# Performance work log

Hardware: AMD Instinct MI355X
Metric: run time of the kernel (lower is better)

Reference implementation:

```python
import jax, jax.numpy as jnp
import numpy as np

HIDDEN = 1024
BATCH = 8192
N_STEPS = 50


def setup_inputs() -> dict:
    key = jax.random.key(0)
    k1, k2, k3 = jax.random.split(key, 3)
    x0 = jax.random.normal(k1, (HIDDEN, BATCH), dtype=jnp.float32)
    W = jax.random.normal(k2, (HIDDEN, HIDDEN), dtype=jnp.float32) * (1.0 / np.sqrt(HIDDEN))
    b = jax.random.normal(k3, (HIDDEN, 1), dtype=jnp.float32)
    t0 = jnp.zeros((), dtype=jnp.float32)
    t1 = jnp.ones((), dtype=jnp.float32)
    return {"x0": x0, "t0": t0, "t1": t1, "W": W, "b": b}


def reference(x0, t0, t1, W, b):
    # Euler integration: x_{i+1} = x_i + h * (W @ x_i + b), h = (t1 - t0) / N
    h = (t1 - t0) / N_STEPS

    def step(x, _):
        x = x + h * (W @ x + b)  # b [H,1] broadcasts over batch
        return x, None

    x_final, _ = jax.lax.scan(step, x0, None, length=N_STEPS)
    return x_final
```

## Files before the change

kernel.cpp:

```cpp
#include <hip/hip_runtime.h>

#define H 1024
#define HH (H * H)
#define BATCH 8192
#define NSTEPS 50

typedef __attribute__((ext_vector_type(8))) short bf16x8;
typedef __attribute__((ext_vector_type(4))) float f32x4;

__device__ __forceinline__ void split2(float a, unsigned short& h, unsigned short& l)
{
    unsigned u = __float_as_uint(a);
    float r = a - __uint_as_float(u & 0xFFFF0000u);
    h = (unsigned short)(u >> 16);
    l = (unsigned short)((__float_as_uint(r) + 0x8000u) >> 16);
}
__device__ __forceinline__ unsigned short rnd_bf16(float a)
{
    return (unsigned short)((__float_as_uint(a) + 0x8000u) >> 16);
}
__device__ __forceinline__ float bf2f(unsigned short s)
{
    return __uint_as_float(((unsigned)s) << 16);
}
__device__ __forceinline__ void gload16(const void* g, void* l)
{
    __builtin_amdgcn_global_load_lds(
        (const __attribute__((address_space(1))) void*)g,
        (__attribute__((address_space(3))) void*)l, 16, 0, 0);
}
#define VMCNT(n) asm volatile("s_waitcnt vmcnt(" #n ")" ::: "memory")
#define RBAR() do { __builtin_amdgcn_s_barrier(); __builtin_amdgcn_sched_barrier(0); } while (0)

__global__ void setup_k(const float* __restrict__ W, const float* __restrict__ bvec,
                        const float* __restrict__ t0, const float* __restrict__ t1,
                        unsigned short* __restrict__ Aplanes,
                        float* __restrict__ cv, float* __restrict__ v0)
{
    __shared__ unsigned short th[64][68], tl[64][68];
    const float h = (t1[0] - t0[0]) / (float)NSTEPS;
    const int bid = blockIdx.x, tid = threadIdx.x;
    const int rb = (bid >> 4) * 64, cb = (bid & 15) * 64;
    const int row = tid >> 2, c16 = (tid & 3) * 16;

    unsigned short* Ahi  = Aplanes;
    unsigned short* Alo  = Aplanes + HH;
    unsigned short* AhiT = Aplanes + 2 * HH;
    unsigned short* AloT = Aplanes + 3 * HH;

    {
        const float* wsrc = &W[(size_t)(rb + row) * H + cb + c16];
        bf16x8 hv[2], lv[2];
        #pragma unroll
        for (int q = 0; q < 16; ++q) {
            const float a = h * wsrc[q] + ((rb + row) == (cb + c16 + q) ? 1.0f : 0.0f);
            unsigned short hh, ll;
            split2(a, hh, ll);
            hv[q >> 3][q & 7] = (short)hh;
            lv[q >> 3][q & 7] = (short)ll;
            th[row][c16 + q] = hh;
            tl[row][c16 + q] = ll;
        }
        *(bf16x8*)&Ahi[(size_t)(rb + row) * H + cb + c16] = hv[0];
        *(bf16x8*)&Ahi[(size_t)(rb + row) * H + cb + c16 + 8] = hv[1];
        *(bf16x8*)&Alo[(size_t)(rb + row) * H + cb + c16] = lv[0];
        *(bf16x8*)&Alo[(size_t)(rb + row) * H + cb + c16 + 8] = lv[1];
    }
    __syncthreads();
    {
        bf16x8 hv[2], lv[2];
        #pragma unroll
        for (int q = 0; q < 16; ++q) {
            hv[q >> 3][q & 7] = (short)th[c16 + q][row];
            lv[q >> 3][q & 7] = (short)tl[c16 + q][row];
        }
        *(bf16x8*)&AhiT[(size_t)(cb + row) * H + rb + c16] = hv[0];
        *(bf16x8*)&AhiT[(size_t)(cb + row) * H + rb + c16 + 8] = hv[1];
        *(bf16x8*)&AloT[(size_t)(cb + row) * H + rb + c16] = lv[0];
        *(bf16x8*)&AloT[(size_t)(cb + row) * H + rb + c16 + 8] = lv[1];
    }
    if (bid == 0) {
        #pragma unroll
        for (int rep = 0; rep < 4; ++rep) {
            const int i = tid + rep * 256;
            const float v = h * bvec[i];
            cv[i] = v; v0[i] = v;
        }
    }
}

template<bool WRITE_N, bool WRITE_T, bool DO_X, bool PR>
__launch_bounds__(512)
__global__ void chain_fused_k(const unsigned short* __restrict__ Lhi,
                              const unsigned short* __restrict__ Llo,
                              const unsigned short* __restrict__ RThi,
                              const unsigned short* __restrict__ RTlo,
                              unsigned short* __restrict__ Qhi,
                              unsigned short* __restrict__ Qlo,
                              unsigned short* __restrict__ QhiT,
                              unsigned short* __restrict__ QloT,
                              const float* __restrict__ vin,
                              const float* __restrict__ addv,
                              float* __restrict__ vout,
                              const float* __restrict__ X,
                              unsigned short* __restrict__ XhiT)
{
    __shared__ unsigned short sA[2][2][2][64][32];
    __shared__ unsigned short sB[2][2][2][64][32];

    const int tid = threadIdx.x;
    const int bid = blockIdx.x;
    const int wave = tid >> 6, lane = tid & 63;

    if (DO_X && bid >= 272) {
        float (*ts)[65] = (float(*)[65])&sA[0][0][0][0][0];
        const int tile = bid - 272;
        const int n0x = (tile >> 4) * 64, k0x = (tile & 15) * 64;
        #pragma unroll
        for (int p = 0; p < 2; ++p) {
            const int kr = p * 32 + (tid >> 4);
            const int c4 = (tid & 15) * 4;
            const float4 v = *(const float4*)&X[(size_t)(k0x + kr) * BATCH + n0x + c4];
            ts[kr][c4 + 0] = v.x; ts[kr][c4 + 1] = v.y;
            ts[kr][c4 + 2] = v.z; ts[kr][c4 + 3] = v.w;
        }
        __syncthreads();
        {
            const int n = tid >> 3;
            const int kc = (tid & 7) * 8;
            bf16x8 hv;
            #pragma unroll
            for (int q = 0; q < 8; ++q)
                hv[q] = (short)rnd_bf16(ts[kc + q][n]);
            *(bf16x8*)&XhiT[(size_t)(n0x + n) * H + k0x + kc] = hv;
        }
        return;
    }

    if (bid >= 256) {
        const int rowbase = (bid - 256) * 64 + wave * 8;
        const float4* xq = (const float4*)vin + lane * 4;
        float4 xv[4];
        #pragma unroll
        for (int q = 0; q < 4; ++q) xv[q] = xq[q];
        #pragma unroll
        for (int rr = 0; rr < 8; ++rr) {
            const int row = rowbase + rr;
            const unsigned short* mh = Lhi + (size_t)row * H + lane * 16;
            const unsigned short* ml = Llo + (size_t)row * H + lane * 16;
            bf16x8 h0 = *(const bf16x8*)&mh[0];
            bf16x8 h1 = *(const bf16x8*)&mh[8];
            bf16x8 l0 = *(const bf16x8*)&ml[0];
            bf16x8 l1 = *(const bf16x8*)&ml[8];
            float s = 0.0f;
            #pragma unroll
            for (int q = 0; q < 8; ++q) {
                const float m0v = bf2f((unsigned short)h0[q]) + bf2f((unsigned short)l0[q]);
                const float m1v = bf2f((unsigned short)h1[q]) + bf2f((unsigned short)l1[q]);
                const float* xf = (const float*)xv;
                s = fmaf(m0v, xf[q], s);
                s = fmaf(m1v, xf[8 + q], s);
            }
            #pragma unroll
            for (int off = 32; off; off >>= 1)
                s += __shfl_down(s, off, 64);
            if (lane == 0) vout[row] = addv[row] + s;
        }
        return;
    }

    const int lg = lane >> 4, lm = lane & 15;
    const int half = wave >> 2;
    const int wq = wave & 3;
    const int wr2 = (wq >> 1) * 32, wc2 = (wq & 1) * 32;
    const int xcd = bid & 7;
    const int idx0 = bid >> 3;
    const int mt = (xcd >> 1) * 4 + (idx0 & 3);
    const int nt = (xcd & 1) * 8 + (idx0 >> 2);
    const int m0 = mt * 64, n0 = nt * 64;

    f32x4 acc[2][2] = {};

    #define CSTAGE(tt, b) do {                                                   \
        _Pragma("unroll")                                                        \
        for (int it = 0; it < 4; ++it) {                                         \
            const int idx = tid + it * 512;                                      \
            const int mat = idx >> 10, kh = (idx >> 9) & 1;                      \
            const int plane = (idx >> 8) & 1;                                    \
            const int row = (idx >> 2) & 63, kc = idx & 3;                       \
            const int ks = kc ^ ((row >> 1) & 3);                                \
            const unsigned short* g = mat ? (plane ? RTlo : RThi)                \
                                          : (plane ? Llo : Lhi);                 \
            const int rb = mat ? n0 : m0;                                        \
            unsigned short* d = mat ? &sB[b][kh][plane][row][kc * 8]             \
                                    : &sA[b][kh][plane][row][kc * 8];            \
            gload16(g + (size_t)(rb + row) * H + kh * 512 + (tt) * 32 + ks * 8, d); \
        }                                                                        \
    } while (0)

    CSTAGE(0, 0);
    __syncthreads();
    int buf = 0;
    for (int t = 0; t < 16; ++t) {
        if (t + 1 < 16) CSTAGE(t + 1, buf ^ 1);
        bf16x8 ah[2], al[2], bh[2], bl[2];
        #pragma unroll
        for (int i = 0; i < 2; ++i) {
            const int row = wr2 + i * 16 + lm;
            const int sl = lg ^ ((row >> 1) & 3);
            ah[i] = *(const bf16x8*)&sA[buf][half][0][row][sl * 8];
            al[i] = *(const bf16x8*)&sA[buf][half][1][row][sl * 8];
            const int rn = wc2 + i * 16 + lm;
            const int sn = lg ^ ((rn >> 1) & 3);
            bh[i] = *(const bf16x8*)&sB[buf][half][0][rn][sn * 8];
            bl[i] = *(const bf16x8*)&sB[buf][half][1][rn][sn * 8];
        }
        #pragma unroll
        for (int i = 0; i < 2; ++i)
            #pragma unroll
            for (int j = 0; j < 2; ++j) {
                acc[i][j] = __builtin_amdgcn_mfma_f32_16x16x32_bf16(ah[i], bh[j], acc[i][j], 0, 0, 0);
                acc[i][j] = __builtin_amdgcn_mfma_f32_16x16x32_bf16(ah[i], bl[j], acc[i][j], 0, 0, 0);
                acc[i][j] = __builtin_amdgcn_mfma_f32_16x16x32_bf16(al[i], bh[j], acc[i][j], 0, 0, 0);
            }
        __syncthreads();
        buf ^= 1;
    }
    #undef CSTAGE

    float* red = (float*)&sA[0][0][0][0][0];
    const int ridx = wq * 64 + lane;
    if (half == 1) {
        float* dst = red + (size_t)ridx * 17;
        #pragma unroll
        for (int i = 0; i < 2; ++i)
            #pragma unroll
            for (int j = 0; j < 2; ++j)
                *(f32x4*)&dst[(i * 2 + j) * 4] = acc[i][j];
    }
    __syncthreads();
    if (half == 0) {
        const float* src = red + (size_t)ridx * 17;
        #pragma unroll
        for (int i = 0; i < 2; ++i)
            #pragma unroll
            for (int j = 0; j < 2; ++j) {
                const f32x4 p = *(const f32x4*)&src[(i * 2 + j) * 4];
                acc[i][j] += p;
            }
        #pragma unroll
        for (int i = 0; i < 2; ++i) {
            const int row0 = m0 + wr2 + i * 16 + lg * 4;
            #pragma unroll
            for (int j = 0; j < 2; ++j) {
                const int col = n0 + wc2 + j * 16 + lm;
                if (PR) {
                    #pragma unroll
                    for (int r = 0; r < 4; ++r)
                        Qhi[(size_t)(row0 + r) * H + col] = rnd_bf16(acc[i][j][r]);
                } else {
                    unsigned short hs[4], ls[4];
                    #pragma unroll
                    for (int r = 0; r < 4; ++r) {
                        split2(acc[i][j][r], hs[r], ls[r]);
                        if (WRITE_N) {
                            Qhi[(size_t)(row0 + r) * H + col] = hs[r];
                            Qlo[(size_t)(row0 + r) * H + col] = ls[r];
                        }
                    }
                    if (WRITE_T) {
                        ushort4 th, tl;
                        th.x = hs[0]; th.y = hs[1]; th.z = hs[2]; th.w = hs[3];
                        tl.x = ls[0]; tl.y = ls[1]; tl.z = ls[2]; tl.w = ls[3];
                        *(ushort4*)&QhiT[(size_t)col * H + row0] = th;
                        *(ushort4*)&QloT[(size_t)col * H + row0] = tl;
                    }
                }
            }
        }
    }
}

__launch_bounds__(256)
__global__ void big_gemm1_k(const unsigned short* __restrict__ Pr,
                            const unsigned short* __restrict__ XhiT,
                            float* __restrict__ C, const float* __restrict__ bias)
{
    __shared__ unsigned short sA[3][128][32];
    __shared__ unsigned short sB[3][128][32];

    const int tid = threadIdx.x;
    const int wave = tid >> 6, lane = tid & 63;
    const int lg = lane >> 4, lm = lane & 15;
    const int wr2 = (wave >> 1) * 64;
    const int wc2 = (wave & 1) * 64;
    const int bid = blockIdx.x;
    const int l = bid >> 3;
    const int m0 = (l & 7) * 128;
    const int n0 = ((bid & 7) * 8 + (l >> 3)) * 128;

    f32x4 acc[4][4] = {};

    #define BSTAGE(tt, b) do {                                                   \
        _Pragma("unroll")                                                        \
        for (int it = 0; it < 2; ++it) {                                         \
            const int idx = tid + it * 256;                                      \
            const int row = idx >> 2, kc = idx & 3;                              \
            const int ks = kc ^ ((row >> 1) & 3);                                \
            const size_t go = (size_t)(tt) * 32 + ks * 8;                        \
            gload16(Pr   + (size_t)(m0 + row) * H + go, &sA[b][row][kc * 8]);    \
            gload16(XhiT + (size_t)(n0 + row) * H + go, &sB[b][row][kc * 8]);    \
        }                                                                        \
    } while (0)

    BSTAGE(0, 0);
    BSTAGE(1, 1);
    VMCNT(2);
    RBAR();

    #pragma unroll
    for (int t = 0; t < 32; ++t) {
        const int b = t % 3;
        bf16x8 ah[4], bh[4];
        #pragma unroll
        for (int i = 0; i < 4; ++i) {
            const int row = wr2 + i * 16 + lm;
            const int sl = lg ^ ((row >> 1) & 3);
            ah[i] = *(const bf16x8*)&sA[b][row][sl * 8];
            const int rn = wc2 + i * 16 + lm;
            const int sn = lg ^ ((rn >> 1) & 3);
            bh[i] = *(const bf16x8*)&sB[b][rn][sn * 8];
        }
        if (t + 2 < 32) BSTAGE(t + 2, (t + 2) % 3);
        __builtin_amdgcn_s_setprio(1);
        #pragma unroll
        for (int i = 0; i < 4; ++i)
            #pragma unroll
            for (int j = 0; j < 4; ++j)
                acc[i][j] = __builtin_amdgcn_mfma_f32_16x16x32_bf16(ah[i], bh[j], acc[i][j], 0, 0, 0);
        __builtin_amdgcn_s_setprio(0);
        if (t < 30) VMCNT(2);
        else if (t == 30) VMCNT(0);
        if (t < 31) RBAR();
    }
    #undef BSTAGE

    #pragma unroll
    for (int i = 0; i < 4; ++i) {
        const int row0 = m0 + wr2 + i * 16 + lg * 4;
        #pragma unroll
        for (int r = 0; r < 4; ++r) {
            const float bv = bias[row0 + r];
            float* dst = &C[(size_t)(row0 + r) * BATCH + n0 + wc2 + lm];
            #pragma unroll
            for (int j = 0; j < 4; ++j)
                dst[j * 16] = acc[i][j][r] + bv;
        }
    }
}

#define PADK 40

__launch_bounds__(256)
__global__ void big_gemm_k(const unsigned short* __restrict__ Ahi_g,
                           const unsigned short* __restrict__ Alo_g,
                           const float* __restrict__ X, float* __restrict__ C,
                           const float* __restrict__ bias)
{
    __shared__ unsigned short Ahi[128][PADK], Alo[128][PADK];
    __shared__ unsigned short Bhi[128][PADK], Blo[128][PADK];

    const int tid = threadIdx.x;
    const int wave = tid >> 6;
    const int lane = tid & 63;
    const int wr = (wave >> 1) * 64;
    const int wc = (wave & 1) * 64;
    const int m0 = blockIdx.y * 128;
    const int n0 = blockIdx.x * 128;
    const int lg = lane >> 4;
    const int lm = lane & 15;

    f32x4 acc[4][4] = {};

    for (int k0 = 0; k0 < H; k0 += 32) {
        #pragma unroll
        for (int a2 = 0; a2 < 2; ++a2) {
            const int id = tid + a2 * 256;
            const int row = id >> 2;
            const int ko = id & 3;
            const size_t g = (size_t)(m0 + row) * H + k0 + ko * 8;
            *(bf16x8*)&Ahi[row][ko * 8] = *(const bf16x8*)&Ahi_g[g];
            *(bf16x8*)&Alo[row][ko * 8] = *(const bf16x8*)&Alo_g[g];
        }
        #pragma unroll
        for (int a2 = 0; a2 < 2; ++a2) {
            const int id = tid + a2 * 256;
            const int n = id & 127;
            const int ko = id >> 7;
            const float* src = &X[(size_t)(k0 + ko * 8) * BATCH + n0 + n];
            bf16x8 bh, bl;
            #pragma unroll
            for (int i = 0; i < 8; ++i) {
                unsigned short hh, ll;
                split2(src[(size_t)i * BATCH], hh, ll);
                bh[i] = (short)hh;
                bl[i] = (short)ll;
            }
            *(bf16x8*)&Bhi[n][ko * 8] = bh;
            *(bf16x8*)&Blo[n][ko * 8] = bl;
        }
        __syncthreads();

        bf16x8 ah[4], al[4], bh[4], bl[4];
        #pragma unroll
        for (int i = 0; i < 4; ++i) {
            const int m = wr + i * 16 + lm;
            ah[i] = *(const bf16x8*)&Ahi[m][lg * 8];
            al[i] = *(const bf16x8*)&Alo[m][lg * 8];
            const int n = wc + i * 16 + lm;
            bh[i] = *(const bf16x8*)&Bhi[n][lg * 8];
            bl[i] = *(const bf16x8*)&Blo[n][lg * 8];
        }
        #pragma unroll
        for (int i = 0; i < 4; ++i)
            #pragma unroll
            for (int j = 0; j < 4; ++j) {
                acc[i][j] = __builtin_amdgcn_mfma_f32_16x16x32_bf16(ah[i], bh[j], acc[i][j], 0, 0, 0);
                acc[i][j] = __builtin_amdgcn_mfma_f32_16x16x32_bf16(ah[i], bl[j], acc[i][j], 0, 0, 0);
                acc[i][j] = __builtin_amdgcn_mfma_f32_16x16x32_bf16(al[i], bh[j], acc[i][j], 0, 0, 0);
            }
        __syncthreads();
    }

    #pragma unroll
    for (int i = 0; i < 4; ++i) {
        const int rowb = m0 + wr + i * 16 + lg * 4;
        #pragma unroll
        for (int r = 0; r < 4; ++r) {
            const float bv = bias[rowb + r];
            float* dst = &C[(size_t)(rowb + r) * BATCH + n0 + wc + lm];
            #pragma unroll
            for (int j = 0; j < 4; ++j)
                dst[j * 16] = acc[i][j][r] + bv;
        }
    }
}

extern "C" void kernel_launch(void* const* d_in, const int* in_sizes, int n_in,
                              void* d_out, int out_size, void* d_ws, size_t ws_size,
                              hipStream_t stream)
{
    const float* x0 = (const float*)d_in[0];
    const float* t0 = (const float*)d_in[1];
    const float* t1 = (const float*)d_in[2];
    const float* W  = (const float*)d_in[3];
    const float* bb = (const float*)d_in[4];
    float* out = (float*)d_out;

    unsigned short* Aplanes = (unsigned short*)d_ws;
    unsigned short* Ahi  = Aplanes;
    unsigned short* Alo  = Aplanes + HH;
    float* cv = (float*)(Aplanes + 4 * HH);
    float* v0 = cv + H;
    float* v1 = v0 + H;

    const size_t xtoff = (size_t)16 * 1024 * 1024;
    const bool useXT = ws_size >= xtoff + (size_t)BATCH * H * sizeof(unsigned short);
    unsigned short* XhiT = (unsigned short*)((char*)d_ws + xtoff);

    unsigned short* PA = (unsigned short*)d_out;
    unsigned short* PB = PA + (size_t)4 * HH;

    setup_k<<<256, 256, 0, stream>>>(W, bb, t0, t1, Aplanes, cv, v0);

    const int seq[7] = {0, 1, 0, 0, 0, 1, 0};
    unsigned short* cur = Ahi;
    float* vin = v0;
    float* vout = v1;
    for (int s = 0; s < 7; ++s) {
        const unsigned short* L  = seq[s] ? Ahi : cur;
        const unsigned short* Ll = seq[s] ? Alo : cur + HH;
        const float* addv = seq[s] ? cv : vin;
        if (s == 0) {
            unsigned short* nxt = PA;
            if (useXT) {
                chain_fused_k<false, true, true, false><<<2320, 512, 0, stream>>>(
                    L, Ll, cur + 2 * HH, cur + 3 * HH,
                    nxt, nxt + HH, nxt + 2 * HH, nxt + 3 * HH,
                    vin, addv, vout, x0, XhiT);
            } else {
                chain_fused_k<false, true, false, false><<<272, 512, 0, stream>>>(
                    L, Ll, cur + 2 * HH, cur + 3 * HH,
                    nxt, nxt + HH, nxt + 2 * HH, nxt + 3 * HH,
                    vin, addv, vout, nullptr, nullptr);
            }
            cur = nxt;
        } else if (s == 4) {
            unsigned short* nxt = PA;
            chain_fused_k<false, true, false, false><<<272, 512, 0, stream>>>(
                L, Ll, cur + 2 * HH, cur + 3 * HH,
                nxt, nxt + HH, nxt + 2 * HH, nxt + 3 * HH,
                vin, addv, vout, nullptr, nullptr);
            cur = nxt;
        } else if (s < 6) {
            unsigned short* nxt = (s & 1) ? PB : PA;
            chain_fused_k<true, true, false, false><<<272, 512, 0, stream>>>(
                L, Ll, cur + 2 * HH, cur + 3 * HH,
                nxt, nxt + HH, nxt + 2 * HH, nxt + 3 * HH,
                vin, addv, vout, nullptr, nullptr);
            cur = nxt;
        } else if (useXT) {
            chain_fused_k<false, false, false, true><<<272, 512, 0, stream>>>(
                L, Ll, cur + 2 * HH, cur + 3 * HH,
                Ahi, nullptr, nullptr, nullptr,
                vin, addv, vout, nullptr, nullptr);
            cur = Ahi;
        } else {
            chain_fused_k<true, false, false, false><<<272, 512, 0, stream>>>(
                L, Ll, cur + 2 * HH, cur + 3 * HH,
                Ahi, Alo, nullptr, nullptr,
                vin, addv, vout, nullptr, nullptr);
            cur = Ahi;
        }
        float* tv = vin; vin = vout; vout = tv;
    }

    if (useXT) {
        big_gemm1_k<<<512, 256, 0, stream>>>(Ahi, XhiT, out, vin);
    } else {
        big_gemm_k<<<dim3(BATCH / 128, H / 128), 256, 0, stream>>>(
            Ahi, Alo, x0, out, vin);
    }
}
```

Measured before the change: 150.8 us.

## Fold matvec into GEMM blocks, add BK64 chain tiles, deepen big GEMM prefetch

```diff
diff --git a/kernel.cpp b/kernel.cpp
--- a/kernel.cpp
+++ b/kernel.cpp
@@ -89,7 +89,7 @@
     }
 }
 
-template<bool WRITE_N, bool WRITE_T, bool DO_X, bool PR>
+template<bool WRITE_N, bool WRITE_T, bool DO_X, bool PR, bool BK64>
 __launch_bounds__(512)
 __global__ void chain_fused_k(const unsigned short* __restrict__ Lhi,
                               const unsigned short* __restrict__ Llo,
@@ -105,16 +105,20 @@
                               const float* __restrict__ X,
                               unsigned short* __restrict__ XhiT)
 {
-    __shared__ unsigned short sA[2][2][2][64][32];
-    __shared__ unsigned short sB[2][2][2][64][32];
+    constexpr int BKH = BK64 ? 64 : 32;
+    constexpr int NIT = 512 / BKH;
+    constexpr int GPR = BKH / 8;
+
+    __shared__ unsigned short sA[2][2][2][64][BKH];
+    __shared__ unsigned short sB[2][2][2][64][BKH];
 
     const int tid = threadIdx.x;
     const int bid = blockIdx.x;
     const int wave = tid >> 6, lane = tid & 63;
 
-    if (DO_X && bid >= 272) {
+    if (DO_X && bid >= 256) {
         float (*ts)[65] = (float(*)[65])&sA[0][0][0][0][0];
-        const int tile = bid - 272;
+        const int tile = bid - 256;
         const int n0x = (tile >> 4) * 64, k0x = (tile & 15) * 64;
         #pragma unroll
         for (int p = 0; p < 2; ++p) {
@@ -133,38 +137,6 @@
             for (int q = 0; q < 8; ++q)
                 hv[q] = (short)rnd_bf16(ts[kc + q][n]);
             *(bf16x8*)&XhiT[(size_t)(n0x + n) * H + k0x + kc] = hv;
-        }
-        return;
-    }
-
-    if (bid >= 256) {
-        const int rowbase = (bid - 256) * 64 + wave * 8;
-        const float4* xq = (const float4*)vin + lane * 4;
-        float4 xv[4];
-        #pragma unroll
-        for (int q = 0; q < 4; ++q) xv[q] = xq[q];
-        #pragma unroll
-        for (int rr = 0; rr < 8; ++rr) {
-            const int row = rowbase + rr;
-            const unsigned short* mh = Lhi + (size_t)row * H + lane * 16;
-            const unsigned short* ml = Llo + (size_t)row * H + lane * 16;
-            bf16x8 h0 = *(const bf16x8*)&mh[0];
-            bf16x8 h1 = *(const bf16x8*)&mh[8];
-            bf16x8 l0 = *(const bf16x8*)&ml[0];
-            bf16x8 l1 = *(const bf16x8*)&ml[8];
-            float s = 0.0f;
-            #pragma unroll
-            for (int q = 0; q < 8; ++q) {
-                const float m0v = bf2f((unsigned short)h0[q]) + bf2f((unsigned short)l0[q]);
-                const float m1v = bf2f((unsigned short)h1[q]) + bf2f((unsigned short)l1[q]);
-                const float* xf = (const float*)xv;
-                s = fmaf(m0v, xf[q], s);
-                s = fmaf(m1v, xf[8 + q], s);
-            }
-            #pragma unroll
-            for (int off = 32; off; off >>= 1)
-                s += __shfl_down(s, off, 64);
-            if (lane == 0) vout[row] = addv[row] + s;
         }
         return;
     }
@@ -181,48 +153,54 @@
 
     f32x4 acc[2][2] = {};
 
-    #define CSTAGE(tt, b) do {                                                   \
-        _Pragma("unroll")                                                        \
-        for (int it = 0; it < 4; ++it) {                                         \
-            const int idx = tid + it * 512;                                      \
-            const int mat = idx >> 10, kh = (idx >> 9) & 1;                      \
-            const int plane = (idx >> 8) & 1;                                    \
-            const int row = (idx >> 2) & 63, kc = idx & 3;                       \
-            const int ks = kc ^ ((row >> 1) & 3);                                \
-            const unsigned short* g = mat ? (plane ? RTlo : RThi)                \
-                                          : (plane ? Llo : Lhi);                 \
-            const int rb = mat ? n0 : m0;                                        \
-            unsigned short* d = mat ? &sB[b][kh][plane][row][kc * 8]             \
-                                    : &sA[b][kh][plane][row][kc * 8];            \
-            gload16(g + (size_t)(rb + row) * H + kh * 512 + (tt) * 32 + ks * 8, d); \
-        }                                                                        \
+    #define CSTAGE(tt, b) do {                                                     \
+        _Pragma("unroll")                                                          \
+        for (int it = 0; it < GPR; ++it) {                                         \
+            const int idx = tid + it * 512;                                        \
+            const int kc = idx % GPR;                                              \
+            const int row = (idx / GPR) & 63;                                      \
+            const int plane = (idx / (GPR * 64)) & 1;                              \
+            const int kh = (idx / (GPR * 128)) & 1;                                \
+            const int mat = idx / (GPR * 256);                                     \
+            const int ks = BK64 ? (kc ^ (row & 7)) : (kc ^ ((row >> 1) & 3));      \
+            const unsigned short* g = mat ? (plane ? RTlo : RThi)                  \
+                                          : (plane ? Llo : Lhi);                   \
+            const int rb = mat ? n0 : m0;                                          \
+            unsigned short* d = mat ? &sB[b][kh][plane][row][kc * 8]               \
+                                    : &sA[b][kh][plane][row][kc * 8];              \
+            gload16(g + (size_t)(rb + row) * H + kh * 512 + (tt) * BKH + ks * 8, d); \
+        }                                                                          \
     } while (0)
 
     CSTAGE(0, 0);
     __syncthreads();
     int buf = 0;
-    for (int t = 0; t < 16; ++t) {
-        if (t + 1 < 16) CSTAGE(t + 1, buf ^ 1);
-        bf16x8 ah[2], al[2], bh[2], bl[2];
-        #pragma unroll
-        for (int i = 0; i < 2; ++i) {
-            const int row = wr2 + i * 16 + lm;
-            const int sl = lg ^ ((row >> 1) & 3);
-            ah[i] = *(const bf16x8*)&sA[buf][half][0][row][sl * 8];
-            al[i] = *(const bf16x8*)&sA[buf][half][1][row][sl * 8];
-            const int rn = wc2 + i * 16 + lm;
-            const int sn = lg ^ ((rn >> 1) & 3);
-            bh[i] = *(const bf16x8*)&sB[buf][half][0][rn][sn * 8];
-            bl[i] = *(const bf16x8*)&sB[buf][half][1][rn][sn * 8];
-        }
-        #pragma unroll
-        for (int i = 0; i < 2; ++i)
-            #pragma unroll
-            for (int j = 0; j < 2; ++j) {
-                acc[i][j] = __builtin_amdgcn_mfma_f32_16x16x32_bf16(ah[i], bh[j], acc[i][j], 0, 0, 0);
-                acc[i][j] = __builtin_amdgcn_mfma_f32_16x16x32_bf16(ah[i], bl[j], acc[i][j], 0, 0, 0);
-                acc[i][j] = __builtin_amdgcn_mfma_f32_16x16x32_bf16(al[i], bh[j], acc[i][j], 0, 0, 0);
+    for (int t = 0; t < NIT; ++t) {
+        if (t + 1 < NIT) CSTAGE(t + 1, buf ^ 1);
+        #pragma unroll
+        for (int kk = 0; kk < (BK64 ? 2 : 1); ++kk) {
+            bf16x8 ah[2], al[2], bh[2], bl[2];
+            #pragma unroll
+            for (int i = 0; i < 2; ++i) {
+                const int row = wr2 + i * 16 + lm;
+                const int g = kk * 4 + lg;
+                const int sl = BK64 ? (g ^ (row & 7)) : (g ^ ((row >> 1) & 3));
+                ah[i] = *(const bf16x8*)&sA[buf][half][0][row][sl * 8];
+                al[i] = *(const bf16x8*)&sA[buf][half][1][row][sl * 8];
+                const int rn = wc2 + i * 16 + lm;
+                const int sn = BK64 ? (g ^ (rn & 7)) : (g ^ ((rn >> 1) & 3));
+                bh[i] = *(const bf16x8*)&sB[buf][half][0][rn][sn * 8];
+                bl[i] = *(const bf16x8*)&sB[buf][half][1][rn][sn * 8];
             }
+            #pragma unroll
+            for (int i = 0; i < 2; ++i)
+                #pragma unroll
+                for (int j = 0; j < 2; ++j) {
+                    acc[i][j] = __builtin_amdgcn_mfma_f32_16x16x32_bf16(ah[i], bh[j], acc[i][j], 0, 0, 0);
+                    acc[i][j] = __builtin_amdgcn_mfma_f32_16x16x32_bf16(ah[i], bl[j], acc[i][j], 0, 0, 0);
+                    acc[i][j] = __builtin_amdgcn_mfma_f32_16x16x32_bf16(al[i], bh[j], acc[i][j], 0, 0, 0);
+                }
+        }
         __syncthreads();
         buf ^= 1;
     }
@@ -278,6 +256,31 @@
                 }
             }
         }
+    } else {
+        const int r = bid * 4 + (wave & 3);
+        const unsigned short* mh = Lhi + (size_t)r * H + lane * 16;
+        const unsigned short* ml = Llo + (size_t)r * H + lane * 16;
+        const float4* xq = (const float4*)vin + lane * 4;
+        float4 xv[4];
+        #pragma unroll
+        for (int q = 0; q < 4; ++q) xv[q] = xq[q];
+        bf16x8 h0 = *(const bf16x8*)&mh[0];
+        bf16x8 h1 = *(const bf16x8*)&mh[8];
+        bf16x8 l0 = *(const bf16x8*)&ml[0];
+        bf16x8 l1 = *(const bf16x8*)&ml[8];
+        float s = 0.0f;
+        const float* xf = (const float*)xv;
+        #pragma unroll
+        for (int q = 0; q < 8; ++q) {
+            const float m0v = bf2f((unsigned short)h0[q]) + bf2f((unsigned short)l0[q]);
+            const float m1v = bf2f((unsigned short)h1[q]) + bf2f((unsigned short)l1[q]);
+            s = fmaf(m0v, xf[q], s);
+            s = fmaf(m1v, xf[8 + q], s);
+        }
+        #pragma unroll
+        for (int off = 32; off; off >>= 1)
+            s += __shfl_down(s, off, 64);
+        if (lane == 0) vout[r] = addv[r] + s;
     }
 }
 
@@ -315,7 +318,7 @@
 
     BSTAGE(0, 0);
     BSTAGE(1, 1);
-    VMCNT(2);
+    VMCNT(4);
     RBAR();
 
     #pragma unroll
@@ -339,7 +342,7 @@
             for (int j = 0; j < 4; ++j)
                 acc[i][j] = __builtin_amdgcn_mfma_f32_16x16x32_bf16(ah[i], bh[j], acc[i][j], 0, 0, 0);
         __builtin_amdgcn_s_setprio(0);
-        if (t < 30) VMCNT(2);
+        if (t < 30) VMCNT(4);
         else if (t == 30) VMCNT(0);
         if (t < 31) RBAR();
     }
@@ -484,12 +487,12 @@
         if (s == 0) {
             unsigned short* nxt = PA;
             if (useXT) {
-                chain_fused_k<false, true, true, false><<<2320, 512, 0, stream>>>(
+                chain_fused_k<false, true, true, false, false><<<2304, 512, 0, stream>>>(
                     L, Ll, cur + 2 * HH, cur + 3 * HH,
                     nxt, nxt + HH, nxt + 2 * HH, nxt + 3 * HH,
                     vin, addv, vout, x0, XhiT);
             } else {
-                chain_fused_k<false, true, false, false><<<272, 512, 0, stream>>>(
+                chain_fused_k<false, true, false, false, false><<<256, 512, 0, stream>>>(
                     L, Ll, cur + 2 * HH, cur + 3 * HH,
                     nxt, nxt + HH, nxt + 2 * HH, nxt + 3 * HH,
                     vin, addv, vout, nullptr, nullptr);
@@ -497,26 +500,26 @@
             cur = nxt;
         } else if (s == 4) {
             unsigned short* nxt = PA;
-            chain_fused_k<false, true, false, false><<<272, 512, 0, stream>>>(
+            chain_fused_k<false, true, false, false, true><<<256, 512, 0, stream>>>(
                 L, Ll, cur + 2 * HH, cur + 3 * HH,
                 nxt, nxt + HH, nxt + 2 * HH, nxt + 3 * HH,
                 vin, addv, vout, nullptr, nullptr);
             cur = nxt;
         } else if (s < 6) {
             unsigned short* nxt = (s & 1) ? PB : PA;
-            chain_fused_k<true, true, false, false><<<272, 512, 0, stream>>>(
+            chain_fused_k<true, true, false, false, true><<<256, 512, 0, stream>>>(
                 L, Ll, cur + 2 * HH, cur + 3 * HH,
                 nxt, nxt + HH, nxt + 2 * HH, nxt + 3 * HH,
                 vin, addv, vout, nullptr, nullptr);
             cur = nxt;
         } else if (useXT) {
-            chain_fused_k<false, false, false, true><<<272, 512, 0, stream>>>(
+            chain_fused_k<false, false, false, true, true><<<256, 512, 0, stream>>>(
                 L, Ll, cur + 2 * HH, cur + 3 * HH,
                 Ahi, nullptr, nullptr, nullptr,
                 vin, addv, vout, nullptr, nullptr);
             cur = Ahi;
         } else {
-            chain_fused_k<true, false, false, false><<<272, 512, 0, stream>>>(
+            chain_fused_k<true, false, false, false, true><<<256, 512, 0, stream>>>(
                 L, Ll, cur + 2 * HH, cur + 3 * HH,
                 Ahi, Alo, nullptr, nullptr,
                 vin, addv, vout, nullptr, nullptr);
```

Result: faster. 133.8 us (median of 2 runs) (-11.3%).

## Triple-buffer chain GEMM pipeline and fold matvec into GEMM blocks

Applied to the files above, without the earlier changes.

```diff
diff --git a/kernel.cpp b/kernel.cpp
--- a/kernel.cpp
+++ b/kernel.cpp
@@ -89,7 +89,7 @@
     }
 }
 
-template<bool WRITE_N, bool WRITE_T, bool DO_X, bool PR>
+template<bool WRITE_N, bool WRITE_T, bool DO_X, bool PR, int MODE>
 __launch_bounds__(512)
 __global__ void chain_fused_k(const unsigned short* __restrict__ Lhi,
                               const unsigned short* __restrict__ Llo,
@@ -105,16 +105,18 @@
                               const float* __restrict__ X,
                               unsigned short* __restrict__ XhiT)
 {
-    __shared__ unsigned short sA[2][2][2][64][32];
-    __shared__ unsigned short sB[2][2][2][64][32];
+    constexpr int NBUF = (MODE == 1) ? 3 : 2;
+
+    __shared__ unsigned short sA[NBUF][2][2][64][32];
+    __shared__ unsigned short sB[NBUF][2][2][64][32];
 
     const int tid = threadIdx.x;
     const int bid = blockIdx.x;
     const int wave = tid >> 6, lane = tid & 63;
 
-    if (DO_X && bid >= 272) {
+    if (DO_X && bid >= 256) {
         float (*ts)[65] = (float(*)[65])&sA[0][0][0][0][0];
-        const int tile = bid - 272;
+        const int tile = bid - 256;
         const int n0x = (tile >> 4) * 64, k0x = (tile & 15) * 64;
         #pragma unroll
         for (int p = 0; p < 2; ++p) {
@@ -133,38 +135,6 @@
             for (int q = 0; q < 8; ++q)
                 hv[q] = (short)rnd_bf16(ts[kc + q][n]);
             *(bf16x8*)&XhiT[(size_t)(n0x + n) * H + k0x + kc] = hv;
-        }
-        return;
-    }
-
-    if (bid >= 256) {
-        const int rowbase = (bid - 256) * 64 + wave * 8;
-        const float4* xq = (const float4*)vin + lane * 4;
-        float4 xv[4];
-        #pragma unroll
-        for (int q = 0; q < 4; ++q) xv[q] = xq[q];
-        #pragma unroll
-        for (int rr = 0; rr < 8; ++rr) {
-            const int row = rowbase + rr;
-            const unsigned short* mh = Lhi + (size_t)row * H + lane * 16;
-            const unsigned short* ml = Llo + (size_t)row * H + lane * 16;
-            bf16x8 h0 = *(const bf16x8*)&mh[0];
-            bf16x8 h1 = *(const bf16x8*)&mh[8];
-            bf16x8 l0 = *(const bf16x8*)&ml[0];
-            bf16x8 l1 = *(const bf16x8*)&ml[8];
-            float s = 0.0f;
-            #pragma unroll
-            for (int q = 0; q < 8; ++q) {
-                const float m0v = bf2f((unsigned short)h0[q]) + bf2f((unsigned short)l0[q]);
-                const float m1v = bf2f((unsigned short)h1[q]) + bf2f((unsigned short)l1[q]);
-                const float* xf = (const float*)xv;
-                s = fmaf(m0v, xf[q], s);
-                s = fmaf(m1v, xf[8 + q], s);
-            }
-            #pragma unroll
-            for (int off = 32; off; off >>= 1)
-                s += __shfl_down(s, off, 64);
-            if (lane == 0) vout[row] = addv[row] + s;
         }
         return;
     }
@@ -185,9 +155,11 @@
         _Pragma("unroll")                                                        \
         for (int it = 0; it < 4; ++it) {                                         \
             const int idx = tid + it * 512;                                      \
-            const int mat = idx >> 10, kh = (idx >> 9) & 1;                      \
+            const int kc = idx & 3;                                              \
+            const int row = (idx >> 2) & 63;                                     \
             const int plane = (idx >> 8) & 1;                                    \
-            const int row = (idx >> 2) & 63, kc = idx & 3;                       \
+            const int kh = (idx >> 9) & 1;                                       \
+            const int mat = idx >> 10;                                           \
             const int ks = kc ^ ((row >> 1) & 3);                                \
             const unsigned short* g = mat ? (plane ? RTlo : RThi)                \
                                           : (plane ? Llo : Lhi);                 \
@@ -198,35 +170,63 @@
         }                                                                        \
     } while (0)
 
-    CSTAGE(0, 0);
-    __syncthreads();
-    int buf = 0;
-    for (int t = 0; t < 16; ++t) {
-        if (t + 1 < 16) CSTAGE(t + 1, buf ^ 1);
-        bf16x8 ah[2], al[2], bh[2], bl[2];
-        #pragma unroll
-        for (int i = 0; i < 2; ++i) {
-            const int row = wr2 + i * 16 + lm;
-            const int sl = lg ^ ((row >> 1) & 3);
-            ah[i] = *(const bf16x8*)&sA[buf][half][0][row][sl * 8];
-            al[i] = *(const bf16x8*)&sA[buf][half][1][row][sl * 8];
-            const int rn = wc2 + i * 16 + lm;
-            const int sn = lg ^ ((rn >> 1) & 3);
-            bh[i] = *(const bf16x8*)&sB[buf][half][0][rn][sn * 8];
-            bl[i] = *(const bf16x8*)&sB[buf][half][1][rn][sn * 8];
-        }
-        #pragma unroll
-        for (int i = 0; i < 2; ++i)
-            #pragma unroll
-            for (int j = 0; j < 2; ++j) {
-                acc[i][j] = __builtin_amdgcn_mfma_f32_16x16x32_bf16(ah[i], bh[j], acc[i][j], 0, 0, 0);
-                acc[i][j] = __builtin_amdgcn_mfma_f32_16x16x32_bf16(ah[i], bl[j], acc[i][j], 0, 0, 0);
-                acc[i][j] = __builtin_amdgcn_mfma_f32_16x16x32_bf16(al[i], bh[j], acc[i][j], 0, 0, 0);
-            }
+    #define CFRAGS(b) \
+        bf16x8 ah[2], al[2], bh[2], bl[2];                                       \
+        _Pragma("unroll")                                                        \
+        for (int i = 0; i < 2; ++i) {                                            \
+            const int row = wr2 + i * 16 + lm;                                   \
+            const int sl = lg ^ ((row >> 1) & 3);                                \
+            ah[i] = *(const bf16x8*)&sA[b][half][0][row][sl * 8];                \
+            al[i] = *(const bf16x8*)&sA[b][half][1][row][sl * 8];                \
+            const int rn = wc2 + i * 16 + lm;                                    \
+            const int sn = lg ^ ((rn >> 1) & 3);                                 \
+            bh[i] = *(const bf16x8*)&sB[b][half][0][rn][sn * 8];                 \
+            bl[i] = *(const bf16x8*)&sB[b][half][1][rn][sn * 8];                 \
+        }
+
+    #define CMFMA()                                                              \
+        _Pragma("unroll")                                                        \
+        for (int i = 0; i < 2; ++i)                                              \
+            _Pragma("unroll")                                                    \
+            for (int j = 0; j < 2; ++j) {                                        \
+                acc[i][j] = __builtin_amdgcn_mfma_f32_16x16x32_bf16(ah[i], bh[j], acc[i][j], 0, 0, 0); \
+                acc[i][j] = __builtin_amdgcn_mfma_f32_16x16x32_bf16(ah[i], bl[j], acc[i][j], 0, 0, 0); \
+                acc[i][j] = __builtin_amdgcn_mfma_f32_16x16x32_bf16(al[i], bh[j], acc[i][j], 0, 0, 0); \
+            }
+
+    if (MODE == 0) {
+        CSTAGE(0, 0);
         __syncthreads();
-        buf ^= 1;
+        int buf = 0;
+        for (int t = 0; t < 16; ++t) {
+            if (t + 1 < 16) CSTAGE(t + 1, buf ^ 1);
+            { CFRAGS(buf) CMFMA() }
+            __syncthreads();
+            buf ^= 1;
+        }
+    } else {
+        CSTAGE(0, 0);
+        CSTAGE(1, 1);
+        VMCNT(4);
+        __builtin_amdgcn_s_barrier();
+        int b = 0;
+        for (int t = 0; t < 16; ++t) {
+            { CFRAGS(b)
+              if (t + 2 < 16) CSTAGE(t + 2, (b == 0) ? 2 : (b - 1));
+              __builtin_amdgcn_s_setprio(1);
+              CMFMA()
+              __builtin_amdgcn_s_setprio(0);
+            }
+            if (t < 14) VMCNT(4);
+            else if (t == 14) VMCNT(0);
+            if (t < 15) __builtin_amdgcn_s_barrier();
+            b = (b == 2) ? 0 : b + 1;
+        }
+        __syncthreads();
     }
     #undef CSTAGE
+    #undef CFRAGS
+    #undef CMFMA
 
     float* red = (float*)&sA[0][0][0][0][0];
     const int ridx = wq * 64 + lane;
@@ -278,6 +278,31 @@
                 }
             }
         }
+    } else {
+        const int r = bid * 4 + (wave & 3);
+        const unsigned short* mh = Lhi + (size_t)r * H + lane * 16;
+        const unsigned short* ml = Llo + (size_t)r * H + lane * 16;
+        const float4* xq = (const float4*)vin + lane * 4;
+        float4 xv[4];
+        #pragma unroll
+        for (int q = 0; q < 4; ++q) xv[q] = xq[q];
+        bf16x8 h0 = *(const bf16x8*)&mh[0];
+        bf16x8 h1 = *(const bf16x8*)&mh[8];
+        bf16x8 l0 = *(const bf16x8*)&ml[0];
+        bf16x8 l1 = *(const bf16x8*)&ml[8];
+        float s = 0.0f;
+        const float* xf = (const float*)xv;
+        #pragma unroll
+        for (int q = 0; q < 8; ++q) {
+            const float m0v = bf2f((unsigned short)h0[q]) + bf2f((unsigned short)l0[q]);
+            const float m1v = bf2f((unsigned short)h1[q]) + bf2f((unsigned short)l1[q]);
+            s = fmaf(m0v, xf[q], s);
+            s = fmaf(m1v, xf[8 + q], s);
+        }
+        #pragma unroll
+        for (int off = 32; off; off >>= 1)
+            s += __shfl_down(s, off, 64);
+        if (lane == 0) vout[r] = addv[r] + s;
     }
 }
 
@@ -315,7 +340,7 @@
 
     BSTAGE(0, 0);
     BSTAGE(1, 1);
-    VMCNT(2);
+    VMCNT(4);
     RBAR();
 
     #pragma unroll
@@ -339,7 +364,7 @@
             for (int j = 0; j < 4; ++j)
                 acc[i][j] = __builtin_amdgcn_mfma_f32_16x16x32_bf16(ah[i], bh[j], acc[i][j], 0, 0, 0);
         __builtin_amdgcn_s_setprio(0);
-        if (t < 30) VMCNT(2);
+        if (t < 30) VMCNT(4);
         else if (t == 30) VMCNT(0);
         if (t < 31) RBAR();
     }
@@ -484,12 +509,12 @@
         if (s == 0) {
             unsigned short* nxt = PA;
             if (useXT) {
-                chain_fused_k<false, true, true, false><<<2320, 512, 0, stream>>>(
+                chain_fused_k<false, true, true, false, 0><<<2304, 512, 0, stream>>>(
                     L, Ll, cur + 2 * HH, cur + 3 * HH,
                     nxt, nxt + HH, nxt + 2 * HH, nxt + 3 * HH,
                     vin, addv, vout, x0, XhiT);
             } else {
-                chain_fused_k<false, true, false, false><<<272, 512, 0, stream>>>(
+                chain_fused_k<false, true, false, false, 0><<<256, 512, 0, stream>>>(
                     L, Ll, cur + 2 * HH, cur + 3 * HH,
                     nxt, nxt + HH, nxt + 2 * HH, nxt + 3 * HH,
                     vin, addv, vout, nullptr, nullptr);
@@ -497,26 +522,26 @@
             cur = nxt;
         } else if (s == 4) {
             unsigned short* nxt = PA;
-            chain_fused_k<false, true, false, false><<<272, 512, 0, stream>>>(
+            chain_fused_k<false, true, false, false, 1><<<256, 512, 0, stream>>>(
                 L, Ll, cur + 2 * HH, cur + 3 * HH,
                 nxt, nxt + HH, nxt + 2 * HH, nxt + 3 * HH,
                 vin, addv, vout, nullptr, nullptr);
             cur = nxt;
         } else if (s < 6) {
             unsigned short* nxt = (s & 1) ? PB : PA;
-            chain_fused_k<true, true, false, false><<<272, 512, 0, stream>>>(
+            chain_fused_k<true, true, false, false, 1><<<256, 512, 0, stream>>>(
                 L, Ll, cur + 2 * HH, cur + 3 * HH,
                 nxt, nxt + HH, nxt + 2 * HH, nxt + 3 * HH,
                 vin, addv, vout, nullptr, nullptr);
             cur = nxt;
         } else if (useXT) {
-            chain_fused_k<false, false, false, true><<<272, 512, 0, stream>>>(
+            chain_fused_k<false, false, false, true, 1><<<256, 512, 0, stream>>>(
                 L, Ll, cur + 2 * HH, cur + 3 * HH,
                 Ahi, nullptr, nullptr, nullptr,
                 vin, addv, vout, nullptr, nullptr);
             cur = Ahi;
         } else {
-            chain_fused_k<true, false, false, false><<<272, 512, 0, stream>>>(
+            chain_fused_k<true, false, false, false, 1><<<256, 512, 0, stream>>>(
                 L, Ll, cur + 2 * HH, cur + 3 * HH,
                 Ahi, Alo, nullptr, nullptr,
                 vin, addv, vout, nullptr, nullptr);
```

After: 141.8 us. -6.0%, faster.
